# Optimization experiments

Hardware: AMD Instinct MI355X
Metric: run time of the kernel (lower is better)

The kernel has to match this reference:

```python
import jax, jax.numpy as jnp
import numpy as np

NUM_POINTS = 18
NUM_DIMS = 4
N = 8_000_000

_LAYER_DIMS = [(16, 1), (64, 16), (256, 64), (64, 256), (16, 64), (NUM_DIMS, 16)]


def setup_inputs() -> dict:
    key = jax.random.key(0)
    ks = jax.random.split(key, 13)
    inp = {"x": jax.random.uniform(ks[0], (N,), dtype=jnp.float32)}
    for i, (o, ii) in enumerate(_LAYER_DIMS):
        s = 1.0 / np.sqrt(ii)
        inp[f"W{i+1}"] = jax.random.uniform(ks[1 + 2 * i], (o, ii), dtype=jnp.float32, minval=-s, maxval=s)
        inp[f"b{i+1}"] = jax.random.uniform(ks[2 + 2 * i], (o,), dtype=jnp.float32, minval=-s, maxval=s)
    return inp


_B = jnp.array([[1.0, 0.0, 0.0], [-2.0, 2.0, 0.0], [1.0, -2.0, 1.0]], dtype=jnp.float32)


def _spline(p, d):
    # p: (3, D) control points, d: (Nb, 1) local parameter
    dd = d[:, 0]
    t = jnp.stack([jnp.ones_like(dd), dd, dd * dd], axis=-1)  # (Nb, 3)
    return (t @ _B) @ p  # (Nb, D)


def _forward(x, W1, b1, W2, b2, W3, b3, W4, b4, W5, b5, W6, b6):
    # control-point MLP on the num_points positions
    pos = jnp.arange(1, NUM_POINTS + 1, dtype=jnp.float32).reshape(NUM_POINTS, 1)
    h = jax.nn.sigmoid(pos @ W1.T + b1)
    h = jax.nn.sigmoid(h @ W2.T + b2)
    h = jax.nn.relu(h @ W3.T + b3)
    h = jax.nn.relu(h @ W4.T + b4)
    h = jax.nn.relu(h @ W5.T + b5)
    P = jnp.cumsum(h @ W6.T + b6, axis=1)  # (NUM_POINTS, NUM_DIMS)

    num_splines = NUM_POINTS - 2
    t_val = x  # (N,)

    def step(carry, xs):
        P_new, probs = carry
        i, P_next = xs
        d = ((t_val * (num_splines - 1) - i) * 0.5)[:, None]  # (N, 1)
        choice = ((d >= 0.0) & (d <= 0.5)).astype(probs.dtype)
        probs = (1.0 - choice) * probs
        P_temp = P_new
        p0 = (P_temp[0] + P_temp[2]) / 4.0 + P_temp[1] / 2.0
        p2 = P_next
        p1 = 2.0 * (P_temp[2] - (p0 + p2) / 4.0)
        P_new = jnp.stack([p0, p1, p2])
        f_prev = _spline(P_temp, d + 0.5)
        f_curr = _spline(P_new, d)
        w = jnp.cos(jnp.pi * d) ** 2 * f_prev + jnp.sin(jnp.pi * d) ** 2 * f_curr
        probs = probs + choice * w
        return (P_new, probs), None

    idx = jnp.arange(num_splines - 1, dtype=jnp.float32)
    P_nexts = P[3:NUM_POINTS]  # (num_splines-1, D)
    probs0 = jnp.zeros((t_val.shape[0], NUM_DIMS), dtype=jnp.float32)
    (_, probs), _ = jax.lax.scan(step, (P[:3], probs0), (idx, P_nexts))
    return probs


def reference(x, W1, b1, W2, b2, W3, b3, W4, b4, W5, b5, W6, b6):
    return _forward(x, W1, b1, W2, b2, W3, b3, W4, b4, W5, b5, W6, b6)
```

## Files before the change

### kernel.cpp

```cpp
#include <hip/hip_runtime.h>
#include <math.h>

#define NPTS    18
#define NDIMS   4
#define NITER   15
#define RSTRIDE 28
#define NBLK    2048

__device__ __forceinline__ float sigm(float v) { return 1.0f / (1.0f + expf(-v)); }
__device__ __forceinline__ float dot4(float4 a, float4 b) {
    return fmaf(a.x, b.x, fmaf(a.y, b.y, fmaf(a.z, b.z, a.w * b.w)));
}

__global__ __launch_bounds__(256) void mlp_kernel(
    const float* __restrict__ W1, const float* __restrict__ b1,
    const float* __restrict__ W2, const float* __restrict__ b2,
    const float* __restrict__ W3, const float* __restrict__ b3,
    const float* __restrict__ W4, const float* __restrict__ b4,
    const float* __restrict__ W5, const float* __restrict__ b5,
    const float* __restrict__ W6, const float* __restrict__ b6,
    float* __restrict__ P)
{
    __shared__ float h1[16], h2[64], h3[256], h4[64], h5[16], z6[4];
    __shared__ float part[256];
    const int t = threadIdx.x;
    const float pos = (float)(blockIdx.x + 1);

    float w1r = W1[t & 15];
    float b1r = b1[t & 15];

    const int o2 = t & 63;
    float4 w2r[4];
    {
        const float4* v = (const float4*)(W2 + o2 * 16);
        #pragma unroll
        for (int k = 0; k < 4; ++k) w2r[k] = v[k];
    }
    float b2r = b2[o2];

    float4 w3r[16];
    {
        const float4* v = (const float4*)(W3 + t * 64);
        #pragma unroll
        for (int k = 0; k < 16; ++k) w3r[k] = v[k];
    }
    float b3r = b3[t];

    const int o4 = t & 63, q4 = t >> 6;
    float4 w4r[16];
    {
        const float4* v = (const float4*)(W4 + o4 * 256 + q4 * 64);
        #pragma unroll
        for (int k = 0; k < 16; ++k) w4r[k] = v[k];
    }
    float b4r = b4[o4];

    const int o5 = t & 15, q5 = (t >> 4) & 3;
    float4 w5r[4];
    {
        const float4* v = (const float4*)(W5 + o5 * 64 + q5 * 16);
        #pragma unroll
        for (int k = 0; k < 4; ++k) w5r[k] = v[k];
    }
    float b5r = b5[o5];

    const int o6 = t & 3;
    float4 w6r[4];
    {
        const float4* v = (const float4*)(W6 + o6 * 16);
        #pragma unroll
        for (int k = 0; k < 4; ++k) w6r[k] = v[k];
    }
    float b6r = b6[o6];

    if (t < 16) h1[t] = sigm(fmaf(w1r, pos, b1r));
    __syncthreads();

    if (t < 64) {
        const float4* h = (const float4*)h1;
        float a = b2r + ((dot4(w2r[0], h[0]) + dot4(w2r[1], h[1])) +
                         (dot4(w2r[2], h[2]) + dot4(w2r[3], h[3])));
        h2[t] = sigm(a);
    }
    __syncthreads();

    {
        const float4* h = (const float4*)h2;
        float a0 = 0.f, a1 = 0.f, a2 = 0.f, a3 = 0.f;
        #pragma unroll
        for (int k = 0; k < 16; k += 4) {
            a0 += dot4(w3r[k + 0], h[k + 0]);
            a1 += dot4(w3r[k + 1], h[k + 1]);
            a2 += dot4(w3r[k + 2], h[k + 2]);
            a3 += dot4(w3r[k + 3], h[k + 3]);
        }
        h3[t] = fmaxf(b3r + ((a0 + a1) + (a2 + a3)), 0.f);
    }
    __syncthreads();

    {
        const float4* h = (const float4*)(h3 + q4 * 64);
        float a0 = 0.f, a1 = 0.f, a2 = 0.f, a3 = 0.f;
        #pragma unroll
        for (int k = 0; k < 16; k += 4) {
            a0 += dot4(w4r[k + 0], h[k + 0]);
            a1 += dot4(w4r[k + 1], h[k + 1]);
            a2 += dot4(w4r[k + 2], h[k + 2]);
            a3 += dot4(w4r[k + 3], h[k + 3]);
        }
        part[t] = (a0 + a1) + (a2 + a3);
    }
    __syncthreads();
    if (t < 64)
        h4[t] = fmaxf(b4r + ((part[t] + part[t + 64]) + (part[t + 128] + part[t + 192])), 0.f);
    __syncthreads();

    if (t < 64) {
        const float4* h = (const float4*)(h4 + q5 * 16);
        part[t] = (dot4(w5r[0], h[0]) + dot4(w5r[1], h[1])) +
                  (dot4(w5r[2], h[2]) + dot4(w5r[3], h[3]));
    }
    __syncthreads();
    if (t < 16)
        h5[t] = fmaxf(b5r + ((part[t] + part[t + 16]) + (part[t + 32] + part[t + 48])), 0.f);
    __syncthreads();

    if (t < 4) {
        const float4* h = (const float4*)h5;
        z6[t] = b6r + ((dot4(w6r[0], h[0]) + dot4(w6r[1], h[1])) +
                       (dot4(w6r[2], h[2]) + dot4(w6r[3], h[3])));
    }
    __syncthreads();

    if (t < 4) {
        float c = 0.f;
        #pragma unroll
        for (int j = 0; j <= 3; ++j) {
            float v = z6[j];
            if (j <= t) c += v;
        }
        P[blockIdx.x * NDIMS + t] = c;
    }
}

__global__ __launch_bounds__(256) void spline_kernel(
    const float* __restrict__ x, const float* __restrict__ P,
    float4* __restrict__ out4, int n)
{
    __shared__ float Praw[NPTS * NDIMS];
    __shared__ float s[NITER * RSTRIDE];
    const int t = threadIdx.x;

    if (t < NPTS * NDIMS) Praw[t] = P[t];
    __syncthreads();

    if (t < NDIMS) {
        const int j = t;
        float P0 = Praw[0 * NDIMS + j];
        float P1 = Praw[1 * NDIMS + j];
        float P2 = Praw[2 * NDIMS + j];
        #pragma unroll
        for (int i = 0; i < NITER; ++i) {
            float Pnext = Praw[(3 + i) * NDIMS + j];
            float p0 = (P0 + P2) * 0.25f + P1 * 0.5f;
            float p2 = Pnext;
            float p1 = 2.0f * (P2 - (p0 + p2) * 0.25f);
            float* row = s + i * RSTRIDE;
            row[0 * 4 + j] = P0; row[1 * 4 + j] = P1; row[2 * 4 + j] = P2;
            row[3 * 4 + j] = p0; row[4 * 4 + j] = p1; row[5 * 4 + j] = p2;
            P0 = p0; P1 = p1; P2 = p2;
        }
    }
    __syncthreads();

    const int stride = NBLK * 256;
    for (int i = blockIdx.x * 256 + t; i < n; i += stride) {
        float u  = x[i] * 15.0f;
        float fi = floorf(u);
        fi = fminf(fmaxf(fi, 0.0f), 14.0f);
        float d  = (u - fi) * 0.5f;

        const float* row = s + (int)fi * RSTRIDE;
        float4 Pt0 = *(const float4*)(row + 0);
        float4 Pt1 = *(const float4*)(row + 4);
        float4 Pt2 = *(const float4*)(row + 8);
        float4 Pn0 = *(const float4*)(row + 12);
        float4 Pn1 = *(const float4*)(row + 16);
        float4 Pn2 = *(const float4*)(row + 20);

        float dp  = d + 0.5f, omp = 0.5f - d;
        float cp0 = omp * omp, cp1 = 2.0f * dp * omp, cp2 = dp * dp;
        float omd = 1.0f - d;
        float cc0 = omd * omd, cc1 = 2.0f * d * omd, cc2 = d * d;

        float wc = fmaf(0.5f, cospif(2.0f * d), 0.5f);

        float4 r;
        {
            float fp = fmaf(cp0, Pt0.x, fmaf(cp1, Pt1.x, cp2 * Pt2.x));
            float fc = fmaf(cc0, Pn0.x, fmaf(cc1, Pn1.x, cc2 * Pn2.x));
            r.x = fmaf(wc, fp - fc, fc);
        }
        {
            float fp = fmaf(cp0, Pt0.y, fmaf(cp1, Pt1.y, cp2 * Pt2.y));
            float fc = fmaf(cc0, Pn0.y, fmaf(cc1, Pn1.y, cc2 * Pn2.y));
            r.y = fmaf(wc, fp - fc, fc);
        }
        {
            float fp = fmaf(cp0, Pt0.z, fmaf(cp1, Pt1.z, cp2 * Pt2.z));
            float fc = fmaf(cc0, Pn0.z, fmaf(cc1, Pn1.z, cc2 * Pn2.z));
            r.z = fmaf(wc, fp - fc, fc);
        }
        {
            float fp = fmaf(cp0, Pt0.w, fmaf(cp1, Pt1.w, cp2 * Pt2.w));
            float fc = fmaf(cc0, Pn0.w, fmaf(cc1, Pn1.w, cc2 * Pn2.w));
            r.w = fmaf(wc, fp - fc, fc);
        }

        out4[i] = r;
    }
}

extern "C" void kernel_launch(void* const* d_in, const int* in_sizes, int n_in,
                              void* d_out, int out_size, void* d_ws, size_t ws_size,
                              hipStream_t stream)
{
    const float* x  = (const float*)d_in[0];
    const float* W1 = (const float*)d_in[1];  const float* b1 = (const float*)d_in[2];
    const float* W2 = (const float*)d_in[3];  const float* b2 = (const float*)d_in[4];
    const float* W3 = (const float*)d_in[5];  const float* b3 = (const float*)d_in[6];
    const float* W4 = (const float*)d_in[7];  const float* b4 = (const float*)d_in[8];
    const float* W5 = (const float*)d_in[9];  const float* b5 = (const float*)d_in[10];
    const float* W6 = (const float*)d_in[11]; const float* b6 = (const float*)d_in[12];

    float* P = (float*)d_ws;
    const int n = in_sizes[0];

    mlp_kernel<<<NPTS, 256, 0, stream>>>(W1, b1, W2, b2, W3, b3, W4, b4, W5, b5, W6, b6, P);

    const int blocks = min(NBLK, (n + 255) / 256);
    spline_kernel<<<blocks, 256, 0, stream>>>(x, P, (float4*)d_out, n);
}
```

Measured before the change: 40.98 us.

## Precompute blended polynomial coefficients and split MLP across 512 threads

The spline table now stores, per segment, collapsed polynomial coefficients (A, B, C plus the difference terms for the blend), so each point needs fewer shared loads and FMAs. The main loop processes 4 elements per thread per chunk, which gives more memory-level parallelism. The MLP kernel uses 512 threads, splitting the 64- and 256-wide reductions to shorten the per-thread dependency chains. Because the kernel is bound by memory traffic (32 MB in, 128 MB out), the arithmetic savings may matter little.

```diff
diff --git a/kernel.cpp b/kernel.cpp
--- a/kernel.cpp
+++ b/kernel.cpp
@@ -6,13 +6,14 @@
 #define NITER   15
 #define RSTRIDE 28
 #define NBLK    2048
+#define CHUNK   1024
 
 __device__ __forceinline__ float sigm(float v) { return 1.0f / (1.0f + expf(-v)); }
 __device__ __forceinline__ float dot4(float4 a, float4 b) {
     return fmaf(a.x, b.x, fmaf(a.y, b.y, fmaf(a.z, b.z, a.w * b.w)));
 }
 
-__global__ __launch_bounds__(256) void mlp_kernel(
+__global__ __launch_bounds__(512) void mlp_kernel(
     const float* __restrict__ W1, const float* __restrict__ b1,
     const float* __restrict__ W2, const float* __restrict__ b2,
     const float* __restrict__ W3, const float* __restrict__ b3,
@@ -22,7 +23,7 @@
     float* __restrict__ P)
 {
     __shared__ float h1[16], h2[64], h3[256], h4[64], h5[16], z6[4];
-    __shared__ float part[256];
+    __shared__ float part[512];
     const int t = threadIdx.x;
     const float pos = (float)(blockIdx.x + 1);
 
@@ -38,30 +39,26 @@
     }
     float b2r = b2[o2];
 
-    float4 w3r[16];
-    {
-        const float4* v = (const float4*)(W3 + t * 64);
-        #pragma unroll
-        for (int k = 0; k < 16; ++k) w3r[k] = v[k];
-    }
-    float b3r = b3[t];
+    const int o3 = t & 255, q3 = t >> 8;
+    float4 w3r[8];
+    {
+        const float4* v = (const float4*)(W3 + o3 * 64 + q3 * 32);
+        #pragma unroll
+        for (int k = 0; k < 8; ++k) w3r[k] = v[k];
+    }
+    float b3r = b3[o3];
 
     const int o4 = t & 63, q4 = t >> 6;
-    float4 w4r[16];
-    {
-        const float4* v = (const float4*)(W4 + o4 * 256 + q4 * 64);
-        #pragma unroll
-        for (int k = 0; k < 16; ++k) w4r[k] = v[k];
+    float4 w4r[8];
+    {
+        const float4* v = (const float4*)(W4 + o4 * 256 + q4 * 32);
+        #pragma unroll
+        for (int k = 0; k < 8; ++k) w4r[k] = v[k];
     }
     float b4r = b4[o4];
 
-    const int o5 = t & 15, q5 = (t >> 4) & 3;
-    float4 w5r[4];
-    {
-        const float4* v = (const float4*)(W5 + o5 * 64 + q5 * 16);
-        #pragma unroll
-        for (int k = 0; k < 4; ++k) w5r[k] = v[k];
-    }
+    const int o5 = t & 15, q5 = (t >> 4) & 15;
+    float4 w5r = *(const float4*)(W5 + o5 * 64 + q5 * 4);
     float b5r = b5[o5];
 
     const int o6 = t & 3;
@@ -85,44 +82,43 @@
     __syncthreads();
 
     {
-        const float4* h = (const float4*)h2;
+        const float4* h = (const float4*)(h2 + q3 * 32);
         float a0 = 0.f, a1 = 0.f, a2 = 0.f, a3 = 0.f;
-        #pragma unroll
-        for (int k = 0; k < 16; k += 4) {
-            a0 += dot4(w3r[k + 0], h[k + 0]);
-            a1 += dot4(w3r[k + 1], h[k + 1]);
-            a2 += dot4(w3r[k + 2], h[k + 2]);
-            a3 += dot4(w3r[k + 3], h[k + 3]);
-        }
-        h3[t] = fmaxf(b3r + ((a0 + a1) + (a2 + a3)), 0.f);
-    }
-    __syncthreads();
-
-    {
-        const float4* h = (const float4*)(h3 + q4 * 64);
+        a0 = dot4(w3r[0], h[0]); a1 = dot4(w3r[1], h[1]);
+        a2 = dot4(w3r[2], h[2]); a3 = dot4(w3r[3], h[3]);
+        a0 += dot4(w3r[4], h[4]); a1 += dot4(w3r[5], h[5]);
+        a2 += dot4(w3r[6], h[6]); a3 += dot4(w3r[7], h[7]);
+        part[t] = (a0 + a1) + (a2 + a3);
+    }
+    __syncthreads();
+    if (t < 256) h3[t] = fmaxf(b3r + part[t] + part[t + 256], 0.f);
+    __syncthreads();
+
+    {
+        const float4* h = (const float4*)(h3 + q4 * 32);
         float a0 = 0.f, a1 = 0.f, a2 = 0.f, a3 = 0.f;
-        #pragma unroll
-        for (int k = 0; k < 16; k += 4) {
-            a0 += dot4(w4r[k + 0], h[k + 0]);
-            a1 += dot4(w4r[k + 1], h[k + 1]);
-            a2 += dot4(w4r[k + 2], h[k + 2]);
-            a3 += dot4(w4r[k + 3], h[k + 3]);
-        }
+        a0 = dot4(w4r[0], h[0]); a1 = dot4(w4r[1], h[1]);
+        a2 = dot4(w4r[2], h[2]); a3 = dot4(w4r[3], h[3]);
+        a0 += dot4(w4r[4], h[4]); a1 += dot4(w4r[5], h[5]);
+        a2 += dot4(w4r[6], h[6]); a3 += dot4(w4r[7], h[7]);
         part[t] = (a0 + a1) + (a2 + a3);
     }
     __syncthreads();
-    if (t < 64)
-        h4[t] = fmaxf(b4r + ((part[t] + part[t + 64]) + (part[t + 128] + part[t + 192])), 0.f);
-    __syncthreads();
-
     if (t < 64) {
-        const float4* h = (const float4*)(h4 + q5 * 16);
-        part[t] = (dot4(w5r[0], h[0]) + dot4(w5r[1], h[1])) +
-                  (dot4(w5r[2], h[2]) + dot4(w5r[3], h[3]));
-    }
-    __syncthreads();
-    if (t < 16)
-        h5[t] = fmaxf(b5r + ((part[t] + part[t + 16]) + (part[t + 32] + part[t + 48])), 0.f);
+        float s = ((part[t] + part[t + 64]) + (part[t + 128] + part[t + 192])) +
+                  ((part[t + 256] + part[t + 320]) + (part[t + 384] + part[t + 448]));
+        h4[t] = fmaxf(b4r + s, 0.f);
+    }
+    __syncthreads();
+
+    if (t < 256) part[t] = dot4(w5r, *(const float4*)(h4 + q5 * 4));
+    __syncthreads();
+    if (t < 16) {
+        float s = 0.f;
+        #pragma unroll
+        for (int q = 0; q < 16; ++q) s += part[t + 16 * q];
+        h5[t] = fmaxf(b5r + s, 0.f);
+    }
     __syncthreads();
 
     if (t < 4) {
@@ -161,63 +157,55 @@
         float P2 = Praw[2 * NDIMS + j];
         #pragma unroll
         for (int i = 0; i < NITER; ++i) {
-            float Pnext = Praw[(3 + i) * NDIMS + j];
+            float Pn = Praw[(3 + i) * NDIMS + j];
             float p0 = (P0 + P2) * 0.25f + P1 * 0.5f;
-            float p2 = Pnext;
+            float p2 = Pn;
             float p1 = 2.0f * (P2 - (p0 + p2) * 0.25f);
+            float Bp = P2 - P0;
+            float Cp = (P0 + P2) - 2.0f * P1;
+            float Bc = 2.0f * (p1 - p0);
+            float Cc = (p0 + p2) - 2.0f * p1;
             float* row = s + i * RSTRIDE;
-            row[0 * 4 + j] = P0; row[1 * 4 + j] = P1; row[2 * 4 + j] = P2;
-            row[3 * 4 + j] = p0; row[4 * 4 + j] = p1; row[5 * 4 + j] = p2;
+            row[0 * 4 + j] = p0;
+            row[1 * 4 + j] = Bc;
+            row[2 * 4 + j] = Cc;
+            row[3 * 4 + j] = Bp - Bc;
+            row[4 * 4 + j] = Cp - Cc;
             P0 = p0; P1 = p1; P2 = p2;
         }
     }
     __syncthreads();
 
-    const int stride = NBLK * 256;
-    for (int i = blockIdx.x * 256 + t; i < n; i += stride) {
-        float u  = x[i] * 15.0f;
-        float fi = floorf(u);
-        fi = fminf(fmaxf(fi, 0.0f), 14.0f);
-        float d  = (u - fi) * 0.5f;
-
-        const float* row = s + (int)fi * RSTRIDE;
-        float4 Pt0 = *(const float4*)(row + 0);
-        float4 Pt1 = *(const float4*)(row + 4);
-        float4 Pt2 = *(const float4*)(row + 8);
-        float4 Pn0 = *(const float4*)(row + 12);
-        float4 Pn1 = *(const float4*)(row + 16);
-        float4 Pn2 = *(const float4*)(row + 20);
-
-        float dp  = d + 0.5f, omp = 0.5f - d;
-        float cp0 = omp * omp, cp1 = 2.0f * dp * omp, cp2 = dp * dp;
-        float omd = 1.0f - d;
-        float cc0 = omd * omd, cc1 = 2.0f * d * omd, cc2 = d * d;
-
-        float wc = fmaf(0.5f, cospif(2.0f * d), 0.5f);
-
-        float4 r;
-        {
-            float fp = fmaf(cp0, Pt0.x, fmaf(cp1, Pt1.x, cp2 * Pt2.x));
-            float fc = fmaf(cc0, Pn0.x, fmaf(cc1, Pn1.x, cc2 * Pn2.x));
-            r.x = fmaf(wc, fp - fc, fc);
+    const int gstride = NBLK * CHUNK;
+    for (int base = blockIdx.x * CHUNK; base < n; base += gstride) {
+        #pragma unroll
+        for (int k = 0; k < 4; ++k) {
+            const int i = base + k * 256 + t;
+            if (i < n) {
+                float u  = x[i] * 15.0f;
+                float fi = floorf(u);
+                fi = fminf(fmaxf(fi, 0.0f), 14.0f);
+                float d  = (u - fi) * 0.5f;
+
+                const float* row = s + (int)fi * RSTRIDE;
+                float4 Ac = *(const float4*)(row + 0);
+                float4 Bc = *(const float4*)(row + 4);
+                float4 Cc = *(const float4*)(row + 8);
+                float4 GB = *(const float4*)(row + 12);
+                float4 GC = *(const float4*)(row + 16);
+
+                float wc  = fmaf(0.5f, cospif(2.0f * d), 0.5f);
+                float wcd = wc * d;
+
+                float4 r;
+                r.x = fmaf(wcd, fmaf(d, GC.x, GB.x), fmaf(d, fmaf(d, Cc.x, Bc.x), Ac.x));
+                r.y = fmaf(wcd, fmaf(d, GC.y, GB.y), fmaf(d, fmaf(d, Cc.y, Bc.y), Ac.y));
+                r.z = fmaf(wcd, fmaf(d, GC.z, GB.z), fmaf(d, fmaf(d, Cc.z, Bc.z), Ac.z));
+                r.w = fmaf(wcd, fmaf(d, GC.w, GB.w), fmaf(d, fmaf(d, Cc.w, Bc.w), Ac.w));
+
+                out4[i] = r;
+            }
         }
-        {
-            float fp = fmaf(cp0, Pt0.y, fmaf(cp1, Pt1.y, cp2 * Pt2.y));
-            float fc = fmaf(cc0, Pn0.y, fmaf(cc1, Pn1.y, cc2 * Pn2.y));
-            r.y = fmaf(wc, fp - fc, fc);
-        }
-        {
-            float fp = fmaf(cp0, Pt0.z, fmaf(cp1, Pt1.z, cp2 * Pt2.z));
-            float fc = fmaf(cc0, Pn0.z, fmaf(cc1, Pn1.z, cc2 * Pn2.z));
-            r.z = fmaf(wc, fp - fc, fc);
-        }
-        {
-            float fp = fmaf(cp0, Pt0.w, fmaf(cp1, Pt1.w, cp2 * Pt2.w));
-            float fc = fmaf(cc0, Pn0.w, fmaf(cc1, Pn1.w, cc2 * Pn2.w));
-            r.w = fmaf(wc, fp - fc, fc);
-        }
-
-        out4[i] = r;
     }
 }
 
@@ -236,8 +224,8 @@
     float* P = (float*)d_ws;
     const int n = in_sizes[0];
 
-    mlp_kernel<<<NPTS, 256, 0, stream>>>(W1, b1, W2, b2, W3, b3, W4, b4, W5, b5, W6, b6, P);
-
-    const int blocks = min(NBLK, (n + 255) / 256);
+    mlp_kernel<<<NPTS, 512, 0, stream>>>(W1, b1, W2, b2, W3, b3, W4, b4, W5, b5, W6, b6, P);
+
+    const int blocks = min(NBLK, (n + CHUNK - 1) / CHUNK);
     spline_kernel<<<blocks, 256, 0, stream>>>(x, P, (float4*)d_out, n);
 }
```

After: 39.13 us. 1.05x faster.
